# Optimization experiments

Measured on AMD Instinct MI355X. Metric: run time of the kernel, lower is better.

Reference implementation:

```python
import jax, jax.numpy as jnp
import numpy as np

N = 50000          # nodes
E = 640000         # edges (before self-loops)
DIM_FEATS = 128
DIM_H = 32
HEADS1 = 8
NUM_CLASS = 16
NEG_SLOPE_ATT = 0.2   # PyG GATv2Conv default negative_slope
NEG_SLOPE_OUT = 0.01  # F.leaky_relu default


def setup_inputs() -> dict:
    key = jax.random.key(0)
    ks = jax.random.split(key, 12)
    s = 0.1
    x = jax.random.normal(ks[0], (N, DIM_FEATS), dtype=jnp.float32)
    edge_index = jax.random.randint(ks[1], (2, E), 0, N, dtype=jnp.int32)
    # GATv2Conv layer 1: dim_feats -> dim_h per head, 8 heads, concat
    W1l = jax.random.normal(ks[2], (DIM_FEATS, HEADS1 * DIM_H), dtype=jnp.float32) * s
    W1r = jax.random.normal(ks[3], (DIM_FEATS, HEADS1 * DIM_H), dtype=jnp.float32) * s
    att1 = jax.random.normal(ks[4], (HEADS1, DIM_H), dtype=jnp.float32) * s
    b1 = jnp.zeros((HEADS1 * DIM_H,), dtype=jnp.float32)
    # GATv2Conv layer 2: 256 -> num_class, 1 head, concat=False
    W2l = jax.random.normal(ks[5], (HEADS1 * DIM_H, NUM_CLASS), dtype=jnp.float32) * s
    W2r = jax.random.normal(ks[6], (HEADS1 * DIM_H, NUM_CLASS), dtype=jnp.float32) * s
    att2 = jax.random.normal(ks[7], (1, NUM_CLASS), dtype=jnp.float32) * s
    b2 = jnp.zeros((NUM_CLASS,), dtype=jnp.float32)
    return {"x": x, "edge_index": edge_index, "W1l": W1l, "W1r": W1r,
            "att1": att1, "b1": b1, "W2l": W2l, "W2r": W2r,
            "att2": att2, "b2": b2}


def _segment_softmax(scores, seg, num_segments):
    # scores: [E, H], seg: [E] destination node ids
    m = jax.ops.segment_max(scores, seg, num_segments=num_segments)  # [N, H]
    e = jnp.exp(scores - m[seg])
    denom = jax.ops.segment_sum(e, seg, num_segments=num_segments)   # [N, H]
    return e / (denom[seg] + 1e-16)


def _gatv2_layer(x, src, dst, Wl, Wr, att, bias, heads, out_ch, concat):
    n = x.shape[0]
    xl = (x @ Wl).reshape(n, heads, out_ch)  # source transform
    xr = (x @ Wr).reshape(n, heads, out_ch)  # target transform
    # per-edge GATv2 score: a^T LeakyReLU(xl[j] + xr[i])
    e = jax.nn.leaky_relu(xl[src] + xr[dst], negative_slope=NEG_SLOPE_ATT)  # [E,H,F]
    alpha = jnp.einsum('ehf,hf->eh', e, att)                                # [E,H]
    alpha = _segment_softmax(alpha, dst, n)
    msg = xl[src] * alpha[:, :, None]                                       # [E,H,F]
    out = jax.ops.segment_sum(msg, dst, num_segments=n)                     # [N,H,F]
    out = out.reshape(n, heads * out_ch) if concat else out.mean(axis=1)
    return out + bias


def reference(x, edge_index, W1l, W1r, att1, b1, W2l, W2r, att2, b2):
    # add_self_loops=True (PyG GATv2Conv default)
    loop = jnp.arange(N, dtype=edge_index.dtype)
    src = jnp.concatenate([edge_index[0], loop])
    dst = jnp.concatenate([edge_index[1], loop])
    # eval mode: all dropouts are identity
    h = _gatv2_layer(x, src, dst, W1l, W1r, att1, b1, HEADS1, DIM_H, concat=True)
    h = jax.nn.elu(h)
    h = _gatv2_layer(h, src, dst, W2l, W2r, att2, b2, 1, NUM_CLASS, concat=False)
    return jax.nn.leaky_relu(h, negative_slope=NEG_SLOPE_OUT)
```

## Files before the change

### kernel.cpp

```cpp
#include <hip/hip_runtime.h>
#include <math.h>

#define NN 50000
#define E0 640000
#define ET 690000
#define F1 128
#define D1 256
#define C2 16
#define NB 196
#define MPAD 50048
#define PADK 136
#define PADK2 264
#define LOG2E 1.4426950408889634f

typedef _Float16 f16x8 __attribute__((ext_vector_type(8)));
typedef _Float16 h2 __attribute__((ext_vector_type(2)));
typedef __attribute__((ext_vector_type(4))) float f32x4;

__device__ __forceinline__ unsigned short f2h(float f) {
  union { _Float16 h; unsigned short u; } c;
  c.h = (_Float16)f;
  return c.u;
}
__device__ __forceinline__ float h2f(unsigned short u) {
  union { unsigned short u; _Float16 h; } c; c.u = u; return (float)c.h;
}
__device__ __forceinline__ h2 u2h2(unsigned u) {
  union { unsigned u; h2 h; } c; c.u = u; return c.h;
}
__device__ __forceinline__ unsigned h22u(h2 h) {
  union { h2 h; unsigned u; } c; c.h = h; return c.u;
}

__global__ __launch_bounds__(256) void k_prep(
    const float* __restrict__ x, const float* __restrict__ Wl,
    const float* __restrict__ Wr, const float* __restrict__ W2l,
    const float* __restrict__ W2r, const int* __restrict__ ei,
    unsigned short* __restrict__ xb, unsigned short* __restrict__ wt,
    unsigned short* __restrict__ wt2, int* __restrict__ deg) {
  const int b = blockIdx.x;
  if (b < 6256) {
    long long i = (long long)(b * 256 + threadIdx.x) * 4;
    if (i >= (long long)MPAD * F1) return;
    float4 v = (i < (long long)NN * F1) ? *(const float4*)&x[i]
                                        : make_float4(0.f, 0.f, 0.f, 0.f);
    ushort4 o;
    o.x = f2h(v.x); o.y = f2h(v.y); o.z = f2h(v.z); o.w = f2h(v.w);
    *(ushort4*)&xb[i] = o;
  } else if (b < 6512) {
    int tid = (b - 6256) * 256 + threadIdx.x;
    int n = tid >> 7, k = tid & 127;
    float v = (n < 256) ? Wl[k * 256 + n] : Wr[k * 256 + (n - 256)];
    wt[tid] = f2h(v);
  } else if (b < 6544) {
    int tid = (b - 6512) * 256 + threadIdx.x;
    int n = tid >> 8, k = tid & 255;
    float v = (n < 16) ? W2l[k * 16 + n] : W2r[k * 16 + (n - 16)];
    wt2[tid] = f2h(v);
  } else {
    int e = (b - 6544) * 256 + threadIdx.x;
    if (e >= ET) return;
    int d = (e < E0) ? ei[E0 + e] : (e - E0);
    atomicAdd(&deg[d], 1);
  }
}

__global__ __launch_bounds__(256) void k_gemm1m(
    const unsigned short* __restrict__ xb, const unsigned short* __restrict__ wt,
    unsigned short* __restrict__ xlh, unsigned short* __restrict__ xrh) {
  __shared__ unsigned short Al[128 * PADK];
  __shared__ unsigned short Bl[128 * PADK];
  const int t = threadIdx.x;
  const int m0 = blockIdx.x * 128;
  const int n0 = blockIdx.y * 128;
  {
    const int r = t >> 4;
    const int c = (t & 15) * 8;
#pragma unroll
    for (int p = 0; p < 8; ++p) {
      const int row = r + p * 16;
      *(float4*)&Al[row * PADK + c] = *(const float4*)&xb[(size_t)(m0 + row) * F1 + c];
      *(float4*)&Bl[row * PADK + c] = *(const float4*)&wt[(size_t)(n0 + row) * F1 + c];
    }
  }
  __syncthreads();
  const int wave = t >> 6, lane = t & 63;
  const int mw = (wave >> 1) * 64, nw = (wave & 1) * 64;
  const int fr = lane & 15, fq = lane >> 4;
  f32x4 acc[4][4] = {};
#pragma unroll
  for (int ks = 0; ks < 4; ++ks) {
    const int ko = ks * 32 + fq * 8;
    f16x8 a[4], b[4];
#pragma unroll
    for (int i = 0; i < 4; ++i)
      a[i] = *(const f16x8*)&Al[(mw + i * 16 + fr) * PADK + ko];
#pragma unroll
    for (int j = 0; j < 4; ++j)
      b[j] = *(const f16x8*)&Bl[(nw + j * 16 + fr) * PADK + ko];
#pragma unroll
    for (int i = 0; i < 4; ++i)
#pragma unroll
      for (int j = 0; j < 4; ++j)
        acc[i][j] = __builtin_amdgcn_mfma_f32_16x16x32_f16(a[i], b[j], acc[i][j], 0, 0, 0);
  }
  unsigned short* outp = (n0 < 256) ? xlh : xrh;
  const int cb = (n0 & 255) + nw + fr;
#pragma unroll
  for (int i = 0; i < 4; ++i) {
    const int gm0 = m0 + mw + i * 16 + fq * 4;
#pragma unroll
    for (int j = 0; j < 4; ++j)
#pragma unroll
      for (int r = 0; r < 4; ++r) {
        const int gm = gm0 + r;
        if (gm < NN) outp[(size_t)gm * D1 + cb + j * 16] = f2h(acc[i][j][r]);
      }
  }
}

__global__ __launch_bounds__(256) void k_scan_part(const int* __restrict__ deg,
                                                   int* __restrict__ part) {
  int i = blockIdx.x * 256 + threadIdx.x;
  int v = (i < NN) ? deg[i] : 0;
  v += __shfl_xor(v, 1);  v += __shfl_xor(v, 2);  v += __shfl_xor(v, 4);
  v += __shfl_xor(v, 8);  v += __shfl_xor(v, 16); v += __shfl_xor(v, 32);
  __shared__ int w[4];
  if ((threadIdx.x & 63) == 0) w[threadIdx.x >> 6] = v;
  __syncthreads();
  if (threadIdx.x == 0) part[blockIdx.x] = w[0] + w[1] + w[2] + w[3];
}

__global__ __launch_bounds__(256) void k_scan_top(int* __restrict__ part,
                                                  int* __restrict__ offs) {
  __shared__ int lds[256];
  int t = threadIdx.x;
  int v = (t < NB) ? part[t] : 0;
  lds[t] = v;
  __syncthreads();
  for (int off = 1; off < 256; off <<= 1) {
    int u = (t >= off) ? lds[t - off] : 0;
    __syncthreads();
    lds[t] += u;
    __syncthreads();
  }
  if (t < NB) part[t] = lds[t] - v;
  if (t == 255) offs[NN] = lds[255];
}

__global__ __launch_bounds__(256) void k_scan_apply(int* __restrict__ deg,
                                                    const int* __restrict__ part,
                                                    int* __restrict__ offs) {
  __shared__ int lds[256];
  int t = threadIdx.x;
  int i = blockIdx.x * 256 + t;
  int v = (i < NN) ? deg[i] : 0;
  lds[t] = v;
  __syncthreads();
  for (int off = 1; off < 256; off <<= 1) {
    int u = (t >= off) ? lds[t - off] : 0;
    __syncthreads();
    lds[t] += u;
    __syncthreads();
  }
  int excl = lds[t] - v + part[blockIdx.x];
  if (i < NN) { offs[i] = excl; deg[i] = excl; }
}

__global__ void k_scatter(const int* __restrict__ ei, int* __restrict__ cur,
                          int* __restrict__ csr) {
  int e = blockIdx.x * 256 + threadIdx.x;
  if (e >= ET) return;
  int s, d;
  if (e < E0) { s = ei[e]; d = ei[E0 + e]; } else { s = d = e - E0; }
  int pos = atomicAdd(&cur[d], 1);
  csr[pos] = s;
}

__global__ __launch_bounds__(256) void k_agg1(
    const unsigned short* __restrict__ xlh, const unsigned short* __restrict__ xrh,
    unsigned short* __restrict__ hb,
    const int* __restrict__ offs, const int* __restrict__ csr,
    const float* __restrict__ att, const float* __restrict__ b1) {
  const int wave = threadIdx.x >> 6;
  const int lane = threadIdx.x & 63;
  const int n = blockIdx.x * 4 + wave;
  const int half = lane >> 5;
  const int sub = lane & 31;
  const int col = sub * 8;
  const uint4 xru = *(const uint4*)&xrh[(size_t)n * D1 + col];
  h2 xr2[4];
  xr2[0] = u2h2(xru.x); xr2[1] = u2h2(xru.y);
  xr2[2] = u2h2(xru.z); xr2[3] = u2h2(xru.w);
  float at8[8];
  *(float4*)&at8[0] = *(const float4*)&att[col];
  *(float4*)&at8[4] = *(const float4*)&att[col + 4];
  h2 ath6[4], ath4[4];
#pragma unroll
  for (int j = 0; j < 4; ++j) {
    ath6[j] = h2{(_Float16)(at8[2 * j] * (0.6f * LOG2E)),
                 (_Float16)(at8[2 * j + 1] * (0.6f * LOG2E))};
    ath4[j] = h2{(_Float16)(at8[2 * j] * (0.4f * LOG2E)),
                 (_Float16)(at8[2 * j + 1] * (0.4f * LOG2E))};
  }
  float l = 0.f;
  h2 acc2[4] = {h2{0, 0}, h2{0, 0}, h2{0, 0}, h2{0, 0}};
  const int beg = offs[n], fin = offs[n + 1];

  auto body = [&](uint4 w) {
    h2 xh[4];
    xh[0] = u2h2(w.x); xh[1] = u2h2(w.y); xh[2] = u2h2(w.z); xh[3] = u2h2(w.w);
    float c = 0.f;
#pragma unroll
    for (int j = 0; j < 4; ++j) {
      h2 v = xh[j] + xr2[j];
      h2 a = u2h2(h22u(v) & 0x7FFF7FFFu);
      c = __builtin_amdgcn_fdot2(v, ath6[j], c, false);
      c = __builtin_amdgcn_fdot2(a, ath4[j], c, false);
    }
    c += __shfl_xor(c, 1);
    c += __shfl_xor(c, 2);
    const float p = exp2f(c);
    l += p;
    const _Float16 ph = (_Float16)p;
    const h2 p2 = h2{ph, ph};
#pragma unroll
    for (int j = 0; j < 4; ++j) acc2[j] += p2 * xh[j];
  };

  int idx = beg + half;
  for (; idx + 4 < fin; idx += 6) {
    const int s0 = csr[idx], s1 = csr[idx + 2], s2 = csr[idx + 4];
    const uint4 w0 = *(const uint4*)&xlh[(size_t)s0 * D1 + col];
    const uint4 w1 = *(const uint4*)&xlh[(size_t)s1 * D1 + col];
    const uint4 w2 = *(const uint4*)&xlh[(size_t)s2 * D1 + col];
    body(w0);
    body(w1);
    body(w2);
  }
  for (; idx < fin; idx += 2) {
    const int s0 = csr[idx];
    const uint4 w0 = *(const uint4*)&xlh[(size_t)s0 * D1 + col];
    body(w0);
  }
  l += __shfl_xor(l, 32);
#pragma unroll
  for (int j = 0; j < 4; ++j) {
    unsigned u = h22u(acc2[j]);
    u = __shfl_xor((int)u, 32);
    acc2[j] += u2h2(u);
  }
  if (half == 0) {
    const float rl = 1.f / (l + 1e-16f);
    float b8[8], o[8];
    *(float4*)&b8[0] = *(const float4*)&b1[col];
    *(float4*)&b8[4] = *(const float4*)&b1[col + 4];
#pragma unroll
    for (int j = 0; j < 4; ++j) {
      o[2 * j]     = (float)acc2[j][0] * rl + b8[2 * j];
      o[2 * j + 1] = (float)acc2[j][1] * rl + b8[2 * j + 1];
    }
#pragma unroll
    for (int k = 0; k < 8; ++k) o[k] = o[k] > 0.f ? o[k] : expm1f(o[k]);
    ushort4 p0, p1;
    p0.x = f2h(o[0]); p0.y = f2h(o[1]); p0.z = f2h(o[2]); p0.w = f2h(o[3]);
    p1.x = f2h(o[4]); p1.y = f2h(o[5]); p1.z = f2h(o[6]); p1.w = f2h(o[7]);
    *(ushort4*)&hb[(size_t)n * D1 + col] = p0;
    *(ushort4*)&hb[(size_t)n * D1 + col + 4] = p1;
  }
}

__global__ __launch_bounds__(256) void k_gemm2m(
    const unsigned short* __restrict__ hb, const unsigned short* __restrict__ wt2,
    unsigned short* __restrict__ h2lh, float* __restrict__ h2r) {
  __shared__ unsigned short Bl[32 * PADK2];
  const int t = threadIdx.x;
  {
    const int n = t >> 3, k0 = (t & 7) * 32;
#pragma unroll
    for (int j = 0; j < 4; ++j)
      *(uint4*)&Bl[n * PADK2 + k0 + j * 8] = *(const uint4*)&wt2[n * 256 + k0 + j * 8];
  }
  __syncthreads();
  const int wave = t >> 6, lane = t & 63;
  const int fr = lane & 15, fq = lane >> 4;
  const int m0 = blockIdx.x * 128 + wave * 32;
  f32x4 acc[2][2] = {};
#pragma unroll
  for (int ks = 0; ks < 8; ++ks) {
    const int ko = ks * 32 + fq * 8;
    f16x8 a[2], b[2];
#pragma unroll
    for (int i = 0; i < 2; ++i) {
      int row = m0 + i * 16 + fr; if (row >= NN) row = NN - 1;
      a[i] = *(const f16x8*)&hb[(size_t)row * D1 + ko];
    }
#pragma unroll
    for (int j = 0; j < 2; ++j)
      b[j] = *(const f16x8*)&Bl[(j * 16 + fr) * PADK2 + ko];
#pragma unroll
    for (int i = 0; i < 2; ++i)
#pragma unroll
      for (int j = 0; j < 2; ++j)
        acc[i][j] = __builtin_amdgcn_mfma_f32_16x16x32_f16(a[i], b[j], acc[i][j], 0, 0, 0);
  }
#pragma unroll
  for (int i = 0; i < 2; ++i) {
    const int gm0 = m0 + i * 16 + fq * 4;
#pragma unroll
    for (int r = 0; r < 4; ++r) {
      const int gm = gm0 + r;
      if (gm < NN) {
        h2lh[(size_t)gm * C2 + fr] = f2h(acc[i][0][r]);
        h2r[(size_t)gm * C2 + fr] = acc[i][1][r];
      }
    }
  }
}

__global__ __launch_bounds__(256) void k_agg2(
    const unsigned short* __restrict__ h2lh, const float* __restrict__ h2r,
    const int* __restrict__ offs, const int* __restrict__ csr,
    const float* __restrict__ att2, const float* __restrict__ b2,
    float* __restrict__ out) {
  const int wave = threadIdx.x >> 6;
  const int lane = threadIdx.x & 63;
  const int n = blockIdx.x * 4 + wave;
  if (n >= NN) return;
  const int c = lane & 15, g = lane >> 4;
  const float xr_v = h2r[(size_t)n * C2 + c];
  const float att_v = att2[c] * LOG2E;
  float l = 0.f, acc = 0.f;
  const int beg = offs[n], fin = offs[n + 1];
  for (int idx = beg + g; idx < fin; idx += 4) {
    int s = csr[idx];
    float xlv = h2f(h2lh[(size_t)s * C2 + c]);
    float v = xlv + xr_v;
    v = fmaxf(v, 0.2f * v);
    float sc0 = v * att_v;
    sc0 += __shfl_xor(sc0, 1);
    sc0 += __shfl_xor(sc0, 2);
    sc0 += __shfl_xor(sc0, 4);
    sc0 += __shfl_xor(sc0, 8);
    float p = exp2f(sc0);
    l += p;
    acc = fmaf(p, xlv, acc);
  }
  l += __shfl_xor(l, 16);   l += __shfl_xor(l, 32);
  acc += __shfl_xor(acc, 16); acc += __shfl_xor(acc, 32);
  float o = acc / (l + 1e-16f) + b2[c];
  o = o > 0.f ? o : 0.01f * o;
  if (lane < 16) out[(size_t)n * C2 + c] = o;
}

extern "C" void kernel_launch(void* const* d_in, const int* in_sizes, int n_in,
                              void* d_out, int out_size, void* d_ws, size_t ws_size,
                              hipStream_t stream) {
  const float* x    = (const float*)d_in[0];
  const int*   ei   = (const int*)d_in[1];
  const float* W1l  = (const float*)d_in[2];
  const float* W1r  = (const float*)d_in[3];
  const float* att1 = (const float*)d_in[4];
  const float* b1   = (const float*)d_in[5];
  const float* W2l  = (const float*)d_in[6];
  const float* W2r  = (const float*)d_in[7];
  const float* att2 = (const float*)d_in[8];
  const float* b2   = (const float*)d_in[9];
  float* out = (float*)d_out;

  unsigned short* xlh = (unsigned short*)d_ws;
  unsigned short* xrh = xlh + (size_t)NN * D1;
  unsigned short* hb  = xrh + (size_t)NN * D1;
  int* deg  = (int*)(hb + (size_t)NN * D1);
  int* offs = deg + NN;
  int* csr  = offs + NN + 1;
  int* part = csr + ET;
  unsigned short* xb = (unsigned short*)(part + NB);
  unsigned short* wt = xb + (size_t)MPAD * F1;
  unsigned short* wt2 = wt + 512 * F1;
  unsigned short* h2lh = xlh;
  float* h2r = (float*)(h2lh + (size_t)NN * C2);

  hipMemsetAsync(deg, 0, NN * sizeof(int), stream);
  k_prep<<<6544 + (ET + 255) / 256, 256, 0, stream>>>(
      x, W1l, W1r, W2l, W2r, ei, xb, wt, wt2, deg);
  k_gemm1m<<<dim3(MPAD / 128, 4), 256, 0, stream>>>(xb, wt, xlh, xrh);
  k_scan_part<<<NB, 256, 0, stream>>>(deg, part);
  k_scan_top<<<1, 256, 0, stream>>>(part, offs);
  k_scan_apply<<<NB, 256, 0, stream>>>(deg, part, offs);
  k_scatter<<<(ET + 255) / 256, 256, 0, stream>>>(ei, deg, csr);
  k_agg1<<<NN / 4, 256, 0, stream>>>(xlh, xrh, hb, offs, csr, att1, b1);
  k_gemm2m<<<(NN + 127) / 128, 256, 0, stream>>>(hb, wt2, h2lh, h2r);
  k_agg2<<<NN / 4, 256, 0, stream>>>(h2lh, h2r, offs, csr, att2, b2, out);
}
```

Measured before the change: 270.5 us.

## Store layer-1 features head-major and split aggregation per head with 16-bit CSR

The first GEMM now writes xl/xr in a head-major [head][node][32] layout. The layer-1 aggregation launches one block per (node group, head), and each wave processes 16 edges in parallel with 4 lanes per edge, instead of 2 edges per wave across the full 256-wide row. CSR source indices are stored as 16-bit values, which halves index traffic; node ids fit because N is below 65536. The aim is more memory-level parallelism for low-degree nodes and lower index bandwidth. The cost is 8x as many waves, each re-reading the CSR and offsets, plus extra shuffle reductions.

```diff
diff --git a/kernel.cpp b/kernel.cpp
--- a/kernel.cpp
+++ b/kernel.cpp
@@ -107,15 +107,19 @@
   unsigned short* outp = (n0 < 256) ? xlh : xrh;
   const int cb = (n0 & 255) + nw + fr;
 #pragma unroll
-  for (int i = 0; i < 4; ++i) {
-    const int gm0 = m0 + mw + i * 16 + fq * 4;
-#pragma unroll
-    for (int j = 0; j < 4; ++j)
+  for (int j = 0; j < 4; ++j) {
+    const int col = cb + j * 16;
+    const int head = col >> 5, f = col & 31;
+    unsigned short* hp = outp + (size_t)head * NN * 32 + f;
+#pragma unroll
+    for (int i = 0; i < 4; ++i) {
+      const int gm0 = m0 + mw + i * 16 + fq * 4;
 #pragma unroll
       for (int r = 0; r < 4; ++r) {
         const int gm = gm0 + r;
-        if (gm < NN) outp[(size_t)gm * D1 + cb + j * 16] = f2h(acc[i][j][r]);
+        if (gm < NN) hp[(size_t)gm * 32] = f2h(acc[i][j][r]);
       }
+    }
   }
 }
 
@@ -168,27 +172,32 @@
 }
 
 __global__ void k_scatter(const int* __restrict__ ei, int* __restrict__ cur,
-                          int* __restrict__ csr) {
+                          unsigned short* __restrict__ csr) {
   int e = blockIdx.x * 256 + threadIdx.x;
   if (e >= ET) return;
   int s, d;
   if (e < E0) { s = ei[e]; d = ei[E0 + e]; } else { s = d = e - E0; }
   int pos = atomicAdd(&cur[d], 1);
-  csr[pos] = s;
+  csr[pos] = (unsigned short)s;
 }
 
 __global__ __launch_bounds__(256) void k_agg1(
     const unsigned short* __restrict__ xlh, const unsigned short* __restrict__ xrh,
     unsigned short* __restrict__ hb,
-    const int* __restrict__ offs, const int* __restrict__ csr,
+    const int* __restrict__ offs, const unsigned short* __restrict__ csr,
     const float* __restrict__ att, const float* __restrict__ b1) {
+  const int b = blockIdx.x;
+  const int head = b & 7;
   const int wave = threadIdx.x >> 6;
+  const int n = (b >> 3) * 4 + wave;
   const int lane = threadIdx.x & 63;
-  const int n = blockIdx.x * 4 + wave;
-  const int half = lane >> 5;
-  const int sub = lane & 31;
-  const int col = sub * 8;
-  const uint4 xru = *(const uint4*)&xrh[(size_t)n * D1 + col];
+  const int g = lane >> 2;
+  const int j4 = lane & 3;
+  const int colh = j4 * 8;
+  const int col = head * 32 + colh;
+  const unsigned short* xlhead = xlh + (size_t)head * NN * 32;
+
+  const uint4 xru = *(const uint4*)&xrh[((size_t)head * NN + n) * 32 + colh];
   h2 xr2[4];
   xr2[0] = u2h2(xru.x); xr2[1] = u2h2(xru.y);
   xr2[2] = u2h2(xru.z); xr2[3] = u2h2(xru.w);
@@ -207,7 +216,9 @@
   h2 acc2[4] = {h2{0, 0}, h2{0, 0}, h2{0, 0}, h2{0, 0}};
   const int beg = offs[n], fin = offs[n + 1];
 
-  auto body = [&](uint4 w) {
+  for (int idx = beg + g; idx < fin; idx += 16) {
+    const int s = csr[idx];
+    const uint4 w = *(const uint4*)&xlhead[(size_t)s * 32 + colh];
     h2 xh[4];
     xh[0] = u2h2(w.x); xh[1] = u2h2(w.y); xh[2] = u2h2(w.z); xh[3] = u2h2(w.w);
     float c = 0.f;
@@ -226,31 +237,18 @@
     const h2 p2 = h2{ph, ph};
 #pragma unroll
     for (int j = 0; j < 4; ++j) acc2[j] += p2 * xh[j];
-  };
-
-  int idx = beg + half;
-  for (; idx + 4 < fin; idx += 6) {
-    const int s0 = csr[idx], s1 = csr[idx + 2], s2 = csr[idx + 4];
-    const uint4 w0 = *(const uint4*)&xlh[(size_t)s0 * D1 + col];
-    const uint4 w1 = *(const uint4*)&xlh[(size_t)s1 * D1 + col];
-    const uint4 w2 = *(const uint4*)&xlh[(size_t)s2 * D1 + col];
-    body(w0);
-    body(w1);
-    body(w2);
-  }
-  for (; idx < fin; idx += 2) {
-    const int s0 = csr[idx];
-    const uint4 w0 = *(const uint4*)&xlh[(size_t)s0 * D1 + col];
-    body(w0);
-  }
-  l += __shfl_xor(l, 32);
+  }
+  l += __shfl_xor(l, 4);  l += __shfl_xor(l, 8);
+  l += __shfl_xor(l, 16); l += __shfl_xor(l, 32);
 #pragma unroll
   for (int j = 0; j < 4; ++j) {
     unsigned u = h22u(acc2[j]);
-    u = __shfl_xor((int)u, 32);
-    acc2[j] += u2h2(u);
-  }
-  if (half == 0) {
+    u = __shfl_xor((int)u, 4);  acc2[j] += u2h2(u);
+    u = h22u(acc2[j]); u = __shfl_xor((int)u, 8);  acc2[j] += u2h2(u);
+    u = h22u(acc2[j]); u = __shfl_xor((int)u, 16); acc2[j] += u2h2(u);
+    u = h22u(acc2[j]); u = __shfl_xor((int)u, 32); acc2[j] += u2h2(u);
+  }
+  if (g == 0) {
     const float rl = 1.f / (l + 1e-16f);
     float b8[8], o[8];
     *(float4*)&b8[0] = *(const float4*)&b1[col];
@@ -265,8 +263,8 @@
     ushort4 p0, p1;
     p0.x = f2h(o[0]); p0.y = f2h(o[1]); p0.z = f2h(o[2]); p0.w = f2h(o[3]);
     p1.x = f2h(o[4]); p1.y = f2h(o[5]); p1.z = f2h(o[6]); p1.w = f2h(o[7]);
-    *(ushort4*)&hb[(size_t)n * D1 + col] = p0;
-    *(ushort4*)&hb[(size_t)n * D1 + col + 4] = p1;
+    *(uint2*)&hb[(size_t)n * D1 + col] = *(uint2*)&p0;
+    *(uint2*)&hb[(size_t)n * D1 + col + 4] = *(uint2*)&p1;
   }
 }
 
@@ -320,7 +318,7 @@
 
 __global__ __launch_bounds__(256) void k_agg2(
     const unsigned short* __restrict__ h2lh, const float* __restrict__ h2r,
-    const int* __restrict__ offs, const int* __restrict__ csr,
+    const int* __restrict__ offs, const unsigned short* __restrict__ csr,
     const float* __restrict__ att2, const float* __restrict__ b2,
     float* __restrict__ out) {
   const int wave = threadIdx.x >> 6;
@@ -373,8 +371,8 @@
   unsigned short* hb  = xrh + (size_t)NN * D1;
   int* deg  = (int*)(hb + (size_t)NN * D1);
   int* offs = deg + NN;
-  int* csr  = offs + NN + 1;
-  int* part = csr + ET;
+  unsigned short* csr = (unsigned short*)(offs + NN + 1);
+  int* part = (int*)(csr + ET + 2);
   unsigned short* xb = (unsigned short*)(part + NB);
   unsigned short* wt = xb + (size_t)MPAD * F1;
   unsigned short* wt2 = wt + 512 * F1;
@@ -389,7 +387,7 @@
   k_scan_top<<<1, 256, 0, stream>>>(part, offs);
   k_scan_apply<<<NB, 256, 0, stream>>>(deg, part, offs);
   k_scatter<<<(ET + 255) / 256, 256, 0, stream>>>(ei, deg, csr);
-  k_agg1<<<NN / 4, 256, 0, stream>>>(xlh, xrh, hb, offs, csr, att1, b1);
+  k_agg1<<<(NN / 4) * 8, 256, 0, stream>>>(xlh, xrh, hb, offs, csr, att1, b1);
   k_gemm2m<<<(NN + 127) / 128, 256, 0, stream>>>(hb, wt2, h2lh, h2r);
   k_agg2<<<NN / 4, 256, 0, stream>>>(h2lh, h2r, offs, csr, att2, b2, out);
 }
```

New measurement: 408.9 us. 1.51x slower.
